# Optimization experiments

Hardware: AMD Instinct MI355X
Metric: run time of the kernel (lower is better)

Reference implementation:

```python
import jax, jax.numpy as jnp
import numpy as np

D = 1024
H = 16
DK = D // H


def setup_inputs() -> dict:
    key = jax.random.key(0)
    ks = jax.random.split(key, 10)
    B, S = 2, 2048
    scale = 1.0 / np.sqrt(D)
    inp = {
        "x": jax.random.normal(ks[0], (B, S, D), dtype=jnp.float32),
        "mask": jax.random.randint(ks[1], (B, S), 0, 2, dtype=jnp.int32),
        "wq": jax.random.normal(ks[2], (D, D), dtype=jnp.float32) * scale,
        "bq": jnp.zeros((D,), dtype=jnp.float32),
        "wk": jax.random.normal(ks[3], (D, D), dtype=jnp.float32) * scale,
        "bk": jnp.zeros((D,), dtype=jnp.float32),
        "wv": jax.random.normal(ks[4], (D, D), dtype=jnp.float32) * scale,
        "bv": jnp.zeros((D,), dtype=jnp.float32),
        "wo": jax.random.normal(ks[5], (D, D), dtype=jnp.float32) * scale,
        "bo": jnp.zeros((D,), dtype=jnp.float32),
    }
    return inp


def reference(x, mask, wq, bq, wk, bk, wv, bv, wo, bo):
    B, S, _ = x.shape
    # torch Linear: y = x @ W.T + b
    def proj(w, b):
        return (jnp.einsum("bsd,ed->bse", x, w) + b).reshape(B, S, H, DK).transpose(0, 2, 1, 3)  # (B,H,S,dk)

    q = proj(wq, bq)
    k = proj(wk, bk)
    v = proj(wv, bv)

    scores = jnp.einsum("bhqd,bhkd->bhqk", q, k) / jnp.sqrt(jnp.float32(DK))  # (B,H,S,S)
    # original: mask.unsqueeze(1).unsqueeze(3) -> (B,1,S,1), masks along the QUERY axis
    m = mask[:, None, :, None]  # (B,1,S,1)
    scores = jnp.where(m == 0, jnp.float32(-1e9), scores)
    attn = jax.nn.softmax(scores, axis=-1)
    ctx = jnp.einsum("bhqk,bhkd->bhqd", attn, v)  # (B,H,S,dk)
    concat = ctx.transpose(0, 2, 1, 3).reshape(B, S, D)
    return jnp.einsum("bsd,ed->bse", concat, wo) + bo
```

## Files before the change

### kernel.cpp

```cpp
#include <hip/hip_runtime.h>
#include <hip/hip_bf16.h>

#define SEQ 2048
#define DM  1024

typedef __attribute__((ext_vector_type(8))) _Float16 f16x8;
typedef __attribute__((ext_vector_type(4)))  float   f32x4;

#define EXP2F(x) __builtin_amdgcn_exp2f(x)

__device__ __forceinline__ ushort f2h(float x) {
    union { _Float16 h; ushort u; } c; c.h = (_Float16)x; return c.u;
}

__device__ __forceinline__ void gload16(const void* g, void* l) {
    __builtin_amdgcn_global_load_lds(
        (const __attribute__((address_space(1))) unsigned*)(uintptr_t)g,
        (__attribute__((address_space(3))) unsigned*)(uintptr_t)l, 16, 0, 0);
}

__global__ __launch_bounds__(256)
void cvt_all(const float* __restrict__ x,  const float* __restrict__ wq,
             const float* __restrict__ wk, const float* __restrict__ wv,
             const float* __restrict__ wo,
             ushort* __restrict__ xH, ushort* __restrict__ wH)
{
    const int NX4 = (2 * SEQ * DM) / 4;
    const int NW4 = (DM * DM) / 4;
    const int total = NX4 + 4 * NW4;
    for (int i = blockIdx.x * 256 + threadIdx.x; i < total; i += gridDim.x * 256) {
        float4 v; ushort4* dst;
        if (i < NX4) {
            v = ((const float4*)x)[i];
            dst = (ushort4*)xH + i;
        } else {
            const int j = i - NX4;
            const int wi = j >> 18;
            const int jo = j & (NW4 - 1);
            const float* ws_ = (wi == 0) ? wq : (wi == 1) ? wk : (wi == 2) ? wv : wo;
            v = ((const float4*)ws_)[jo];
            dst = (ushort4*)wH + j;
        }
        ushort4 h;
        h.x = f2h(v.x); h.y = f2h(v.y); h.z = f2h(v.z); h.w = f2h(v.w);
        *dst = h;
    }
}

template<int BM, int BN, int WM, int WN, int MODE>
__global__ __launch_bounds__(WM * WN * 64)
void gemm5(const ushort* __restrict__ A, const ushort* __restrict__ B,
           const float* __restrict__ b0, const float* __restrict__ b1,
           const float* __restrict__ b2,
           ushort* __restrict__ QH, ushort* __restrict__ KH,
           ushort* __restrict__ VH, float* __restrict__ outf, int nmt)
{
    constexpr int NW  = WM * WN;
    constexpr int PR  = BM / WM, PC = BN / WN;
    constexpr int MR  = PR / 16, NR = PC / 16, MH = MR / 2;
    constexpr int APW = (BM / 8) / NW;
    constexpr int BPW = (BN / 8) / NW;
    constexpr int NL  = APW + BPW;
    constexpr int NT  = DM / 64;

    __shared__ ushort A_lds[2][BM * 64];
    __shared__ ushort B_lds[2][BN * 64];

    const int tid = threadIdx.x, w = tid >> 6, lane = tid & 63;
    const int nwg = gridDim.x, q8 = nwg >> 3;
    const int wg  = (blockIdx.x & 7) * q8 + (blockIdx.x >> 3);
    const int m0  = (wg % nmt) * BM, n0 = (wg / nmt) * BN;
    const int wm  = w / WN, wn = w % WN;

    auto stage = [&](int buf, int kt) {
        const int k0 = kt * 64;
#pragma unroll
        for (int j = 0; j < APW; ++j) {
            const int s   = w * APW + j;
            const int row = s * 8 + (lane >> 3);
            const int cl  = (lane & 7) ^ (row & 7);
            gload16(A + (size_t)(m0 + row) * DM + k0 + cl * 8,
                    &A_lds[buf][s * 512]);
        }
#pragma unroll
        for (int j = 0; j < BPW; ++j) {
            const int s   = w * BPW + j;
            const int row = s * 8 + (lane >> 3);
            const int cl  = (lane & 7) ^ (row & 7);
            gload16(B + (size_t)(n0 + row) * DM + k0 + cl * 8,
                    &B_lds[buf][s * 512]);
        }
    };

    f32x4 acc[MR][NR];
#pragma unroll
    for (int i = 0; i < MR; ++i)
#pragma unroll
        for (int j = 0; j < NR; ++j) acc[i][j] = f32x4{0.f, 0.f, 0.f, 0.f};

    stage(0, 0);
    stage(1, 1);

    for (int t = 0; t < NT; ++t) {
        const int buf = t & 1;
        if (t == NT - 1) asm volatile("s_waitcnt vmcnt(0)" ::: "memory");
        else             asm volatile("s_waitcnt vmcnt(8)" ::: "memory");
        __builtin_amdgcn_sched_barrier(0);
        __builtin_amdgcn_s_barrier();

        frag_read:;
        f16x8 bf_[NR][2];
#pragma unroll
        for (int nf = 0; nf < NR; ++nf) {
            const int r = wn * PC + nf * 16 + (lane & 15);
#pragma unroll
            for (int kb = 0; kb < 2; ++kb) {
                const int c = kb * 4 + (lane >> 4);
                bf_[nf][kb] = *(const f16x8*)&B_lds[buf][r * 64 + ((c ^ (r & 7)) << 3)];
            }
        }
#pragma unroll
        for (int qm = 0; qm < 2; ++qm) {
            f16x8 af_[MH][2];
#pragma unroll
            for (int mf = 0; mf < MH; ++mf) {
                const int r = wm * PR + qm * (PR / 2) + mf * 16 + (lane & 15);
#pragma unroll
                for (int kb = 0; kb < 2; ++kb) {
                    const int c = kb * 4 + (lane >> 4);
                    af_[mf][kb] = *(const f16x8*)&A_lds[buf][r * 64 + ((c ^ (r & 7)) << 3)];
                }
            }
            __builtin_amdgcn_s_setprio(1);
#pragma unroll
            for (int kb = 0; kb < 2; ++kb)
#pragma unroll
                for (int mf = 0; mf < MH; ++mf)
#pragma unroll
                    for (int nf = 0; nf < NR; ++nf)
                        acc[qm * MH + mf][nf] = __builtin_amdgcn_mfma_f32_16x16x32_f16(
                            af_[mf][kb], bf_[nf][kb], acc[qm * MH + mf][nf], 0, 0, 0);
            __builtin_amdgcn_s_setprio(0);
        }
        __builtin_amdgcn_sched_barrier(0);
        __builtin_amdgcn_s_barrier();
        __builtin_amdgcn_sched_barrier(0);
        if (t + 2 < NT) stage(buf, t + 2);
    }

#pragma unroll
    for (int mf = 0; mf < MR; ++mf)
#pragma unroll
        for (int nf = 0; nf < NR; ++nf) {
            const int col  = n0 + wn * PC + nf * 16 + (lane & 15);
            const int row0 = m0 + wm * PR + mf * 16 + ((lane >> 4) << 2);
            f32x4 v = acc[mf][nf];
            if constexpr (MODE == 1) {
                float4 o;
                o.x = v[0] + b0[row0 + 0];
                o.y = v[1] + b0[row0 + 1];
                o.z = v[2] + b0[row0 + 2];
                o.w = v[3] + b0[row0 + 3];
                *(float4*)&outf[(size_t)col * DM + row0] = o;
            } else {
                const int sel = row0 >> 10;
                const int e = row0 & 1023;
                const int b = col >> 11, s = col & 2047;
                const int h = e >> 6, dk = e & 63;
                const float* bp = (sel == 0) ? b0 : (sel == 1) ? b1 : b2;
                const float sc = (sel == 0) ? 0.125f * 1.44269504089f : 1.0f;
                const float v0 = (v[0] + bp[e + 0]) * sc;
                const float v1 = (v[1] + bp[e + 1]) * sc;
                const float v2 = (v[2] + bp[e + 2]) * sc;
                const float v3 = (v[3] + bp[e + 3]) * sc;
                const int bh = b * 16 + h;
                ushort4 hv;
                hv.x = f2h(v0); hv.y = f2h(v1); hv.z = f2h(v2); hv.w = f2h(v3);
                if (sel == 0) {
                    const size_t off = ((size_t)bh * SEQ + s) * 64 + dk;
                    *(ushort4*)&QH[off] = hv;
                } else if (sel == 1) {
                    const size_t off = ((size_t)bh * SEQ + s) * 64 + dk;
                    *(ushort4*)&KH[off] = hv;
                } else {
                    const size_t o0 = ((size_t)bh * 64 + dk) * SEQ + s;
                    VH[o0]           = hv.x;
                    VH[o0 + SEQ]     = hv.y;
                    VH[o0 + 2 * SEQ] = hv.z;
                    VH[o0 + 3 * SEQ] = hv.w;
                }
            }
        }
}

__global__ __launch_bounds__(512, 2)
void attn_k(const ushort* __restrict__ QH, const ushort* __restrict__ KH,
            const ushort* __restrict__ VH, const int* __restrict__ mask,
            ushort* __restrict__ ch)
{
    __shared__ ushort Ks[64 * 64];
    __shared__ ushort Vs[64 * 64];
    __shared__ ushort Ps[8][32 * 64];

    const int t = threadIdx.x, w = t >> 6, lane = t & 63;
    const int bh = blockIdx.x >> 3, qt = blockIdx.x & 7;
    const int b = bh >> 4, h = bh & 15;
    const int q0 = qt * 256 + w * 32;
    const size_t base = (size_t)bh * SEQ * 64;

    f16x8 qf[2][2];
#pragma unroll
    for (int nf = 0; nf < 2; ++nf)
#pragma unroll
        for (int kb = 0; kb < 2; ++kb) {
            const size_t off = base + (size_t)(q0 + nf * 16 + (lane & 15)) * 64
                             + kb * 32 + ((lane >> 4) << 3);
            qf[nf][kb] = *(const f16x8*)&QH[off];
        }

    int msk[2];
#pragma unroll
    for (int nf = 0; nf < 2; ++nf)
        msk[nf] = mask[b * SEQ + q0 + nf * 16 + (lane & 15)];

    float m_run[2] = {-1e30f, -1e30f}, l_run[2] = {0.f, 0.f};
    f32x4 acc[4][2];
#pragma unroll
    for (int df = 0; df < 4; ++df)
#pragma unroll
        for (int nf = 0; nf < 2; ++nf) acc[df][nf] = f32x4{0.f, 0.f, 0.f, 0.f};

    f16x8 sK, sV;
    const int sr = t >> 3, scc = t & 7;
    auto stage_load = [&](int kt) {
        sK = *(const f16x8*)&KH[base + (size_t)(kt * 64 + sr) * 64 + scc * 8];
        sV = *(const f16x8*)&VH[base + (size_t)sr * SEQ + kt * 64 + scc * 8];
    };
    auto stage_write = [&]() {
        const int ph = scc ^ (sr & 7);
        *(f16x8*)&Ks[sr * 64 + ph * 8] = sK;
        *(f16x8*)&Vs[sr * 64 + ph * 8] = sV;
    };

    stage_load(0); stage_write();
    __syncthreads();

    for (int kt = 0; kt < SEQ / 64; ++kt) {
        if (kt < SEQ / 64 - 1) stage_load(kt + 1);

        f32x4 st[4][2];
#pragma unroll
        for (int mf = 0; mf < 4; ++mf)
#pragma unroll
            for (int nf = 0; nf < 2; ++nf) st[mf][nf] = f32x4{0.f, 0.f, 0.f, 0.f};
        __builtin_amdgcn_s_setprio(1);
#pragma unroll
        for (int mf = 0; mf < 4; ++mf) {
            const int r = mf * 16 + (lane & 15);
            const int cb = lane >> 4;
#pragma unroll
            for (int kb = 0; kb < 2; ++kb) {
                const int c = kb * 4 + cb;
                const int p = c ^ (r & 7);
                f16x8 kf = *(const f16x8*)&Ks[r * 64 + p * 8];
#pragma unroll
                for (int nf = 0; nf < 2; ++nf)
                    st[mf][nf] = __builtin_amdgcn_mfma_f32_16x16x32_f16(kf, qf[nf][kb], st[mf][nf], 0, 0, 0);
            }
        }
        __builtin_amdgcn_s_setprio(0);

#pragma unroll
        for (int nf = 0; nf < 2; ++nf) {
            if (msk[nf] == 0) {
#pragma unroll
                for (int mf = 0; mf < 4; ++mf) st[mf][nf] = f32x4{0.f, 0.f, 0.f, 0.f};
            }
            float mx = -1e30f;
#pragma unroll
            for (int mf = 0; mf < 4; ++mf)
#pragma unroll
                for (int r4 = 0; r4 < 4; ++r4) mx = fmaxf(mx, st[mf][nf][r4]);
            mx = fmaxf(mx, __shfl_xor(mx, 16));
            mx = fmaxf(mx, __shfl_xor(mx, 32));
            if (!__all(mx - m_run[nf] <= 8.0f)) {
                const float mnew = fmaxf(m_run[nf], mx);
                const float corr = EXP2F(m_run[nf] - mnew);
                m_run[nf] = mnew;
                l_run[nf] *= corr;
#pragma unroll
                for (int df = 0; df < 4; ++df)
#pragma unroll
                    for (int r4 = 0; r4 < 4; ++r4) acc[df][nf][r4] *= corr;
            }
            float ss = 0.f;
#pragma unroll
            for (int mf = 0; mf < 4; ++mf)
#pragma unroll
                for (int r4 = 0; r4 < 4; ++r4) {
                    const float p = EXP2F(st[mf][nf][r4] - m_run[nf]);
                    st[mf][nf][r4] = p; ss += p;
                }
            ss += __shfl_xor(ss, 16);
            ss += __shfl_xor(ss, 32);
            l_run[nf] += ss;
        }

#pragma unroll
        for (int nf = 0; nf < 2; ++nf) {
            const int q = nf * 16 + (lane & 15);
#pragma unroll
            for (int mf = 0; mf < 4; ++mf) {
                const int key0 = mf * 16 + ((lane >> 4) << 2);
                ushort4 hv;
                hv.x = f2h(st[mf][nf][0]);
                hv.y = f2h(st[mf][nf][1]);
                hv.z = f2h(st[mf][nf][2]);
                hv.w = f2h(st[mf][nf][3]);
                const int c = key0 >> 3, sub = key0 & 7;
                const int p = c ^ (q & 7);
                *(ushort4*)&Ps[w][q * 64 + p * 8 + sub] = hv;
            }
        }

        f16x8 pf[2][2];
#pragma unroll
        for (int nf = 0; nf < 2; ++nf) {
            const int q = nf * 16 + (lane & 15);
            const int cb = lane >> 4;
#pragma unroll
            for (int kb = 0; kb < 2; ++kb) {
                const int c = kb * 4 + cb;
                const int p = c ^ (q & 7);
                pf[nf][kb] = *(const f16x8*)&Ps[w][q * 64 + p * 8];
            }
        }
        __builtin_amdgcn_s_setprio(1);
#pragma unroll
        for (int df = 0; df < 4; ++df) {
            const int r = df * 16 + (lane & 15);
            const int cb = lane >> 4;
#pragma unroll
            for (int kb = 0; kb < 2; ++kb) {
                const int c = kb * 4 + cb;
                const int p = c ^ (r & 7);
                f16x8 vf = *(const f16x8*)&Vs[r * 64 + p * 8];
#pragma unroll
                for (int nf = 0; nf < 2; ++nf)
                    acc[df][nf] = __builtin_amdgcn_mfma_f32_16x16x32_f16(vf, pf[nf][kb], acc[df][nf], 0, 0, 0);
            }
        }
        __builtin_amdgcn_s_setprio(0);

        __syncthreads();
        if (kt < SEQ / 64 - 1) {
            stage_write();
            __syncthreads();
        }
    }

#pragma unroll
    for (int nf = 0; nf < 2; ++nf) {
        const float inv = 1.0f / l_run[nf];
        const int s = q0 + nf * 16 + (lane & 15);
#pragma unroll
        for (int df = 0; df < 4; ++df) {
            const int e0 = h * 64 + df * 16 + ((lane >> 4) << 2);
            ushort4 hv;
            hv.x = f2h(acc[df][nf][0] * inv);
            hv.y = f2h(acc[df][nf][1] * inv);
            hv.z = f2h(acc[df][nf][2] * inv);
            hv.w = f2h(acc[df][nf][3] * inv);
            *(ushort4*)&ch[(size_t)(b * SEQ + s) * DM + e0] = hv;
        }
    }
}

extern "C" void kernel_launch(void* const* d_in, const int* in_sizes, int n_in,
                              void* d_out, int out_size, void* d_ws, size_t ws_size,
                              hipStream_t stream)
{
    const float* x  = (const float*)d_in[0];
    const int* mask = (const int*)d_in[1];
    const float* wq = (const float*)d_in[2];
    const float* bq = (const float*)d_in[3];
    const float* wk = (const float*)d_in[4];
    const float* bk = (const float*)d_in[5];
    const float* wv = (const float*)d_in[6];
    const float* bv = (const float*)d_in[7];
    const float* wo = (const float*)d_in[8];
    const float* bo = (const float*)d_in[9];
    float* out = (float*)d_out;

    const size_t M1 = 1024 * 1024;
    ushort* W = (ushort*)d_ws;
    ushort* xH = W;
    ushort* wH = W + 4 * M1;
    ushort* QH = W + 8 * M1;
    ushort* KH = W + 12 * M1;
    ushort* VH = W + 16 * M1;

    cvt_all<<<2048, 256, 0, stream>>>(x, wq, wk, wv, wo, xH, wH);

    gemm5<384, 128, 4, 2, 0><<<256, 512, 0, stream>>>(
        wH, xH, bq, bk, bv, QH, KH, VH, nullptr, 8);

    attn_k<<<256, 512, 0, stream>>>(QH, KH, VH, mask, xH);

    gemm5<128, 128, 2, 2, 1><<<256, 256, 0, stream>>>(
        wH + 3 * M1, xH, bo, nullptr, nullptr,
        nullptr, nullptr, nullptr, out, 8);
}
```

Before: 115.9 us.

## Halve attention query tile per wave and double grid to 512 blocks

```diff
diff --git a/kernel.cpp b/kernel.cpp
--- a/kernel.cpp
+++ b/kernel.cpp
@@ -60,7 +60,6 @@
     constexpr int MR  = PR / 16, NR = PC / 16, MH = MR / 2;
     constexpr int APW = (BM / 8) / NW;
     constexpr int BPW = (BN / 8) / NW;
-    constexpr int NL  = APW + BPW;
     constexpr int NT  = DM / 64;
 
     __shared__ ushort A_lds[2][BM * 64];
@@ -108,7 +107,6 @@
         __builtin_amdgcn_sched_barrier(0);
         __builtin_amdgcn_s_barrier();
 
-        frag_read:;
         f16x8 bf_[NR][2];
 #pragma unroll
         for (int nf = 0; nf < NR; ++nf) {
@@ -200,35 +198,27 @@
 {
     __shared__ ushort Ks[64 * 64];
     __shared__ ushort Vs[64 * 64];
-    __shared__ ushort Ps[8][32 * 64];
+    __shared__ ushort Ps[8][16 * 64];
 
     const int t = threadIdx.x, w = t >> 6, lane = t & 63;
-    const int bh = blockIdx.x >> 3, qt = blockIdx.x & 7;
+    const int wg = (blockIdx.x & 7) * 64 + (blockIdx.x >> 3);
+    const int bh = wg >> 4, qt = wg & 15;
     const int b = bh >> 4, h = bh & 15;
-    const int q0 = qt * 256 + w * 32;
+    const int q0 = qt * 128 + w * 16;
     const size_t base = (size_t)bh * SEQ * 64;
-
-    f16x8 qf[2][2];
-#pragma unroll
-    for (int nf = 0; nf < 2; ++nf)
-#pragma unroll
-        for (int kb = 0; kb < 2; ++kb) {
-            const size_t off = base + (size_t)(q0 + nf * 16 + (lane & 15)) * 64
-                             + kb * 32 + ((lane >> 4) << 3);
-            qf[nf][kb] = *(const f16x8*)&QH[off];
-        }
-
-    int msk[2];
-#pragma unroll
-    for (int nf = 0; nf < 2; ++nf)
-        msk[nf] = mask[b * SEQ + q0 + nf * 16 + (lane & 15)];
-
-    float m_run[2] = {-1e30f, -1e30f}, l_run[2] = {0.f, 0.f};
-    f32x4 acc[4][2];
-#pragma unroll
-    for (int df = 0; df < 4; ++df)
-#pragma unroll
-        for (int nf = 0; nf < 2; ++nf) acc[df][nf] = f32x4{0.f, 0.f, 0.f, 0.f};
+    const int lq = lane & 15, cb = lane >> 4;
+
+    f16x8 qf[2];
+#pragma unroll
+    for (int kb = 0; kb < 2; ++kb)
+        qf[kb] = *(const f16x8*)&QH[base + (size_t)(q0 + lq) * 64 + kb * 32 + cb * 8];
+
+    const int msk = mask[b * SEQ + q0 + lq];
+
+    float m_run = -1e30f, l_run = 0.f;
+    f32x4 acc[4];
+#pragma unroll
+    for (int df = 0; df < 4; ++df) acc[df] = f32x4{0.f, 0.f, 0.f, 0.f};
 
     f16x8 sK, sV;
     const int sr = t >> 3, scc = t & 7;
@@ -248,106 +238,85 @@
     for (int kt = 0; kt < SEQ / 64; ++kt) {
         if (kt < SEQ / 64 - 1) stage_load(kt + 1);
 
-        f32x4 st[4][2];
-#pragma unroll
-        for (int mf = 0; mf < 4; ++mf)
-#pragma unroll
-            for (int nf = 0; nf < 2; ++nf) st[mf][nf] = f32x4{0.f, 0.f, 0.f, 0.f};
+        f32x4 st[4];
+#pragma unroll
+        for (int mf = 0; mf < 4; ++mf) st[mf] = f32x4{0.f, 0.f, 0.f, 0.f};
         __builtin_amdgcn_s_setprio(1);
 #pragma unroll
         for (int mf = 0; mf < 4; ++mf) {
-            const int r = mf * 16 + (lane & 15);
-            const int cb = lane >> 4;
+            const int r = mf * 16 + lq;
 #pragma unroll
             for (int kb = 0; kb < 2; ++kb) {
-                const int c = kb * 4 + cb;
-                const int p = c ^ (r & 7);
+                const int p = (kb * 4 + cb) ^ (r & 7);
                 f16x8 kf = *(const f16x8*)&Ks[r * 64 + p * 8];
-#pragma unroll
-                for (int nf = 0; nf < 2; ++nf)
-                    st[mf][nf] = __builtin_amdgcn_mfma_f32_16x16x32_f16(kf, qf[nf][kb], st[mf][nf], 0, 0, 0);
+                st[mf] = __builtin_amdgcn_mfma_f32_16x16x32_f16(kf, qf[kb], st[mf], 0, 0, 0);
             }
         }
         __builtin_amdgcn_s_setprio(0);
 
-#pragma unroll
-        for (int nf = 0; nf < 2; ++nf) {
-            if (msk[nf] == 0) {
-#pragma unroll
-                for (int mf = 0; mf < 4; ++mf) st[mf][nf] = f32x4{0.f, 0.f, 0.f, 0.f};
+        {
+            if (msk == 0) {
+#pragma unroll
+                for (int mf = 0; mf < 4; ++mf) st[mf] = f32x4{0.f, 0.f, 0.f, 0.f};
             }
             float mx = -1e30f;
 #pragma unroll
             for (int mf = 0; mf < 4; ++mf)
 #pragma unroll
-                for (int r4 = 0; r4 < 4; ++r4) mx = fmaxf(mx, st[mf][nf][r4]);
-            mx = fmaxf(mx, __shfl_xor(mx, 16));
-            mx = fmaxf(mx, __shfl_xor(mx, 32));
-            if (!__all(mx - m_run[nf] <= 8.0f)) {
-                const float mnew = fmaxf(m_run[nf], mx);
-                const float corr = EXP2F(m_run[nf] - mnew);
-                m_run[nf] = mnew;
-                l_run[nf] *= corr;
+                for (int r4 = 0; r4 < 4; ++r4) mx = fmaxf(mx, st[mf][r4]);
+            if (!__all(mx - m_run <= 8.0f)) {
+                mx = fmaxf(mx, __shfl_xor(mx, 16));
+                mx = fmaxf(mx, __shfl_xor(mx, 32));
+                const float mnew = fmaxf(m_run, mx);
+                const float corr = EXP2F(m_run - mnew);
+                m_run = mnew;
+                l_run *= corr;
 #pragma unroll
                 for (int df = 0; df < 4; ++df)
 #pragma unroll
-                    for (int r4 = 0; r4 < 4; ++r4) acc[df][nf][r4] *= corr;
+                    for (int r4 = 0; r4 < 4; ++r4) acc[df][r4] *= corr;
             }
             float ss = 0.f;
 #pragma unroll
             for (int mf = 0; mf < 4; ++mf)
 #pragma unroll
                 for (int r4 = 0; r4 < 4; ++r4) {
-                    const float p = EXP2F(st[mf][nf][r4] - m_run[nf]);
-                    st[mf][nf][r4] = p; ss += p;
+                    const float p = EXP2F(st[mf][r4] - m_run);
+                    st[mf][r4] = p; ss += p;
                 }
             ss += __shfl_xor(ss, 16);
             ss += __shfl_xor(ss, 32);
-            l_run[nf] += ss;
-        }
-
-#pragma unroll
-        for (int nf = 0; nf < 2; ++nf) {
-            const int q = nf * 16 + (lane & 15);
-#pragma unroll
-            for (int mf = 0; mf < 4; ++mf) {
-                const int key0 = mf * 16 + ((lane >> 4) << 2);
-                ushort4 hv;
-                hv.x = f2h(st[mf][nf][0]);
-                hv.y = f2h(st[mf][nf][1]);
-                hv.z = f2h(st[mf][nf][2]);
-                hv.w = f2h(st[mf][nf][3]);
-                const int c = key0 >> 3, sub = key0 & 7;
-                const int p = c ^ (q & 7);
-                *(ushort4*)&Ps[w][q * 64 + p * 8 + sub] = hv;
-            }
-        }
-
-        f16x8 pf[2][2];
-#pragma unroll
-        for (int nf = 0; nf < 2; ++nf) {
-            const int q = nf * 16 + (lane & 15);
-            const int cb = lane >> 4;
+            l_run += ss;
+        }
+
+#pragma unroll
+        for (int mf = 0; mf < 4; ++mf) {
+            const int key0 = mf * 16 + (cb << 2);
+            ushort4 hv;
+            hv.x = f2h(st[mf][0]);
+            hv.y = f2h(st[mf][1]);
+            hv.z = f2h(st[mf][2]);
+            hv.w = f2h(st[mf][3]);
+            const int c = key0 >> 3, sub = key0 & 7;
+            const int p = c ^ (lq & 7);
+            *(ushort4*)&Ps[w][lq * 64 + p * 8 + sub] = hv;
+        }
+
+        f16x8 pf[2];
+#pragma unroll
+        for (int kb = 0; kb < 2; ++kb) {
+            const int p = (kb * 4 + cb) ^ (lq & 7);
+            pf[kb] = *(const f16x8*)&Ps[w][lq * 64 + p * 8];
+        }
+        __builtin_amdgcn_s_setprio(1);
+#pragma unroll
+        for (int df = 0; df < 4; ++df) {
+            const int r = df * 16 + lq;
 #pragma unroll
             for (int kb = 0; kb < 2; ++kb) {
-                const int c = kb * 4 + cb;
-                const int p = c ^ (q & 7);
-                pf[nf][kb] = *(const f16x8*)&Ps[w][q * 64 + p * 8];
-            }
-        }
-        __builtin_amdgcn_s_setprio(1);
-#pragma unroll
-        for (int df = 0; df < 4; ++df) {
-            const int r = df * 16 + (lane & 15);
-            const int cb = lane >> 4;
-#pragma unroll
-            for (int kb = 0; kb < 2; ++kb) {
-                const int c = kb * 4 + cb;
-                const int p = c ^ (r & 7);
+                const int p = (kb * 4 + cb) ^ (r & 7);
                 f16x8 vf = *(const f16x8*)&Vs[r * 64 + p * 8];
-#pragma unroll
-                for (int nf = 0; nf < 2; ++nf)
-                    acc[df][nf] = __builtin_amdgcn_mfma_f32_16x16x32_f16(vf, pf[nf][kb], acc[df][nf], 0, 0, 0);
+                acc[df] = __builtin_amdgcn_mfma_f32_16x16x32_f16(vf, pf[kb], acc[df], 0, 0, 0);
             }
         }
         __builtin_amdgcn_s_setprio(0);
@@ -359,18 +328,17 @@
         }
     }
 
-#pragma unroll
-    for (int nf = 0; nf < 2; ++nf) {
-        const float inv = 1.0f / l_run[nf];
-        const int s = q0 + nf * 16 + (lane & 15);
+    {
+        const float inv = 1.0f / l_run;
+        const int s = q0 + lq;
 #pragma unroll
         for (int df = 0; df < 4; ++df) {
-            const int e0 = h * 64 + df * 16 + ((lane >> 4) << 2);
+            const int e0 = h * 64 + df * 16 + (cb << 2);
             ushort4 hv;
-            hv.x = f2h(acc[df][nf][0] * inv);
-            hv.y = f2h(acc[df][nf][1] * inv);
-            hv.z = f2h(acc[df][nf][2] * inv);
-            hv.w = f2h(acc[df][nf][3] * inv);
+            hv.x = f2h(acc[df][0] * inv);
+            hv.y = f2h(acc[df][1] * inv);
+            hv.z = f2h(acc[df][2] * inv);
+            hv.w = f2h(acc[df][3] * inv);
             *(ushort4*)&ch[(size_t)(b * SEQ + s) * DM + e0] = hv;
         }
     }
@@ -405,7 +373,7 @@
     gemm5<384, 128, 4, 2, 0><<<256, 512, 0, stream>>>(
         wH, xH, bq, bk, bv, QH, KH, VH, nullptr, 8);
 
-    attn_k<<<256, 512, 0, stream>>>(QH, KH, VH, mask, xH);
+    attn_k<<<512, 512, 0, stream>>>(QH, KH, VH, mask, xH);
 
     gemm5<128, 128, 2, 2, 1><<<256, 256, 0, stream>>>(
         wH + 3 * M1, xH, bo, nullptr, nullptr,
```

New measurement: 113.8 us. No clear change (-1.8%).
